# Optimization experiments

Measured on AMD Instinct MI355X. Metric: run time of the kernel, lower is better.

Reference implementation:

```python
import jax, jax.numpy as jnp
import numpy as np

N = 50000          # nodes
E = 1_600_000      # edges (avg degree 32)
IN_N, IN_E = 16, 1 # fc_encoder hardwired input dims
H = 128            # per-layer out_node/out_edge channels (out//2 = 64 inner)
BN_EPS = 1e-5


def setup_inputs() -> dict:
    key = jax.random.key(0)
    ks = jax.random.split(key, 32)
    d = {}
    d["x"] = jax.random.normal(ks[0], (N, IN_N), jnp.float32)
    d["edge_attr"] = jax.random.normal(ks[1], (E, IN_E), jnp.float32)
    d["edge_index"] = jax.random.randint(ks[2], (2, E), 0, N)
    i = 3
    for l, (ni, ei) in enumerate([(IN_N, IN_E), (H, H)]):
        s_n = 1.0 / np.sqrt(ni)
        s_e = 1.0 / np.sqrt(ei)
        s_h = 1.0 / np.sqrt(H)
        d[f"l{l}_Wn"] = jax.random.normal(ks[i], (H // 2, ni), jnp.float32) * s_n; i += 1
        d[f"l{l}_We"] = jax.random.normal(ks[i], (H // 2, ei), jnp.float32) * s_e; i += 1
        d[f"l{l}_Wfn"] = jax.random.normal(ks[i], (H, H), jnp.float32) * s_h; i += 1
        d[f"l{l}_bfn"] = jax.random.normal(ks[i], (H,), jnp.float32) * s_h; i += 1
        d[f"l{l}_Wfe"] = jax.random.normal(ks[i], (H, H), jnp.float32) * s_h; i += 1
        d[f"l{l}_bfe"] = jax.random.normal(ks[i], (H,), jnp.float32) * s_h; i += 1
        d[f"l{l}_g"] = jax.random.uniform(ks[i], (H,), jnp.float32, 0.5, 1.5); i += 1
        d[f"l{l}_b"] = jax.random.normal(ks[i], (H,), jnp.float32) * 0.1; i += 1
        d[f"l{l}_rm"] = jax.random.normal(ks[i], (H,), jnp.float32) * 0.1; i += 1
        d[f"l{l}_rv"] = jax.random.uniform(ks[i], (H,), jnp.float32, 0.5, 1.5); i += 1
    return d


def _layer(x, ea, src, dst, Wn, We, Wfn, bfn, Wfe, bfe, g, b, rm, rv):
    # NodeEdgeInteraction_node (eval mode: dropout = identity)
    n1 = jax.nn.relu(x @ Wn.T)            # [N, H/2]
    e1 = jax.nn.relu(ea @ We.T)           # [E, H/2]
    # edge_updater: cat([n1[src] + n1[dst], e1])
    e2 = jnp.concatenate([n1[src] + n1[dst], e1], axis=-1)      # [E, H]
    # propagate: message = e1, sum-aggregate at destination (edge_index[1])
    agg = jax.ops.segment_sum(e1, dst, num_segments=x.shape[0])  # [N, H/2]
    n2 = jnp.concatenate([agg, n1], axis=-1)                     # [N, H]
    n2 = jax.nn.relu(n2 @ Wfn.T + bfn)
    e2 = jax.nn.relu(e2 @ Wfe.T + bfe)
    # BatchNorm1d (eval: running stats)
    n2 = (n2 - rm) * jax.lax.rsqrt(rv + BN_EPS) * g + b
    return n2, e2


def reference(x, edge_attr, edge_index,
              l0_Wn, l0_We, l0_Wfn, l0_bfn, l0_Wfe, l0_bfe, l0_g, l0_b, l0_rm, l0_rv,
              l1_Wn, l1_We, l1_Wfn, l1_bfn, l1_Wfe, l1_bfe, l1_g, l1_b, l1_rm, l1_rv):
    src, dst = edge_index[0], edge_index[1]
    x, edge_attr = _layer(x, edge_attr, src, dst,
                          l0_Wn, l0_We, l0_Wfn, l0_bfn, l0_Wfe, l0_bfe,
                          l0_g, l0_b, l0_rm, l0_rv)
    x, edge_attr = _layer(x, edge_attr, src, dst,
                          l1_Wn, l1_We, l1_Wfn, l1_bfn, l1_Wfe, l1_bfe,
                          l1_g, l1_b, l1_rm, l1_rv)
    return x  # GNNEncoder returns node embeddings only
```

## Files before the change

kernel.cpp:

```cpp
#include <hip/hip_runtime.h>

typedef unsigned short u16;
typedef __attribute__((ext_vector_type(8))) short short8;
typedef __attribute__((ext_vector_type(4))) float floatx4;

#define NN 50000
#define NE 1600000
#define BN_EPS 1e-5f
#define TPB 8

#define LDS_BARRIER() asm volatile("s_waitcnt lgkmcnt(0)\n\ts_barrier" ::: "memory")

__device__ __forceinline__ float bfu(u16 u) {
    union { unsigned u32; float f; } v; v.u32 = ((unsigned)u) << 16; return v.f;
}
__device__ __forceinline__ u16 f2bf(float f) {
    union { float f; unsigned u; } v; v.f = f;
    unsigned r = v.u + 0x7FFFu + ((v.u >> 16) & 1u);
    return (u16)(r >> 16);
}
__device__ __forceinline__ float ldf(const void* p, int i, int m) {
    return m ? ((const float*)p)[i] : bfu(((const u16*)p)[i]);
}

__global__ __launch_bounds__(256) void k_cvtw(const u16* __restrict__ x,
                                              const void* __restrict__ W0, const void* __restrict__ W1,
                                              const void* __restrict__ W2, const void* __restrict__ W3,
                                              const void* __restrict__ W4,
                                              const void* __restrict__ We0raw,
                                              u16* __restrict__ dst, float* __restrict__ PN,
                                              int* __restrict__ mode) {
    int t = threadIdx.x;
    __shared__ float sred[4];
    float mx = 0.f;
    for (int i = t; i < 4096; i += 256) mx = fmaxf(mx, fabsf(bfu(x[i])));
#pragma unroll
    for (int o = 32; o > 0; o >>= 1) mx = fmaxf(mx, __shfl_down(mx, o));
    if ((t & 63) == 0) sred[t >> 6] = mx;
    __syncthreads();
    float m2 = fmaxf(fmaxf(sred[0], sred[1]), fmaxf(sred[2], sred[3]));
    int m = (m2 > 1e4f) ? 1 : 0;
    if (blockIdx.x == 0 && t == 0) mode[0] = m;
    if (blockIdx.x == 256) {
        if (t < 128) {
            float p = 0.f, n = 0.f;
            for (int k = 0; k < 64; k++) {
                float w = ldf(We0raw, k, m);
                float wf = ldf(W0, t * 128 + 64 + k, m);
                p += fmaxf(w, 0.f) * wf;
                n += fminf(w, 0.f) * wf;
            }
            PN[t] = p; PN[128 + t] = n;
        }
        return;
    }
    int i = blockIdx.x * 256 + t;
    const void* src; int off;
    if (i < 16384)      { src = W0; off = i; }
    else if (i < 24576) { src = W1; off = i - 16384; }
    else if (i < 40960) { src = W2; off = i - 24576; }
    else if (i < 49152) { src = W3; off = i - 40960; }
    else                { src = W4; off = i - 49152; }
    dst[i] = m ? f2bf(((const float*)src)[off]) : ((const u16*)src)[off];
}

__global__ __launch_bounds__(256) void k_enc0h(const void* __restrict__ x, const void* __restrict__ Wn,
                                               u16* __restrict__ n1, const int* __restrict__ ei,
                                               const void* __restrict__ ea,
                                               float* __restrict__ sp, float* __restrict__ sn,
                                               const int* __restrict__ mf) {
    int b = blockIdx.x;
    int t = threadIdx.x;
    int m = mf[0];
    if (b >= 3125) {
        int e = (b - 3125) * 256 + t;
        float a = ldf(ea, e, m);
        int d = ei[NE + e];
        if (a > 0.f) atomicAdd(sp + d, a);
        else if (a < 0.f) atomicAdd(sn + d, a);
        return;
    }
    __shared__ float Wns[64 * 17];
    __shared__ float xsh[16][17];
    int n0 = b * 16;
    for (int i = t; i < 1024; i += 256) Wns[(i >> 4) * 17 + (i & 15)] = ldf(Wn, i, m);
    xsh[t >> 4][t & 15] = ldf(x, n0 * 16 + t, m);
    __syncthreads();
    int c = t & 63, ng = t >> 6;
    float a0 = 0.f, a1 = 0.f, a2 = 0.f, a3 = 0.f;
#pragma unroll
    for (int k = 0; k < 16; k++) {
        float wv = Wns[c * 17 + k];
        a0 += xsh[ng * 4 + 0][k] * wv;
        a1 += xsh[ng * 4 + 1][k] * wv;
        a2 += xsh[ng * 4 + 2][k] * wv;
        a3 += xsh[ng * 4 + 3][k] * wv;
    }
    n1[(n0 + ng * 4 + 0) * 64 + c] = f2bf(fmaxf(a0, 0.f));
    n1[(n0 + ng * 4 + 1) * 64 + c] = f2bf(fmaxf(a1, 0.f));
    n1[(n0 + ng * 4 + 2) * 64 + c] = f2bf(fmaxf(a2, 0.f));
    n1[(n0 + ng * 4 + 3) * 64 + c] = f2bf(fmaxf(a3, 0.f));
}

__global__ __launch_bounds__(256) void k_node_l0(
    const u16* __restrict__ n1l0, const float* __restrict__ sp, const float* __restrict__ sn,
    const void* __restrict__ We0, const u16* __restrict__ Wfn0c, const void* __restrict__ bfn0,
    const void* __restrict__ g0, const void* __restrict__ b0,
    const void* __restrict__ rm0, const void* __restrict__ rv0,
    const u16* __restrict__ Wn1c, u16* __restrict__ n1l1, const int* __restrict__ mf) {
    int m = mf[0];
    __shared__ __align__(16) u16 fs[64][136];
    __shared__ __align__(16) u16 xs[64][136];
    int t = threadIdx.x;
    int n0 = blockIdx.x * 64;
    {
        int col = t & 127;
        int rbase = t >> 7;
        float wp = 0.f, wn = 0.f;
        if (col < 64) { float w0 = ldf(We0, col, m); wp = fmaxf(w0, 0.f); wn = fminf(w0, 0.f); }
#pragma unroll
        for (int i = 0; i < 32; i++) {
            int row = rbase + 2 * i;
            int n = n0 + row;
            float v = 0.f;
            if (n < NN) v = (col < 64) ? (wp * sp[n] + wn * sn[n]) : bfu(n1l0[n * 64 + col - 64]);
            fs[row][col] = f2bf(v);
        }
    }
    __syncthreads();
    int lane = t & 63, w = t >> 6, q = lane >> 4, nidx = lane & 15;
    {
        const u16* ar = &fs[w * 16 + nidx][0];
        short8 a0 = *(const short8*)&ar[q * 8];
        short8 a1 = *(const short8*)&ar[32 + q * 8];
        short8 a2 = *(const short8*)&ar[64 + q * 8];
        short8 a3 = *(const short8*)&ar[96 + q * 8];
#pragma unroll
        for (int jt = 0; jt < 8; jt++) {
            int j = jt * 16 + nidx;
            const u16* wr = Wfn0c + j * 128;
            floatx4 acc = {0.f, 0.f, 0.f, 0.f};
            acc = __builtin_amdgcn_mfma_f32_16x16x32_bf16(a0, *(const short8*)&wr[q * 8], acc, 0, 0, 0);
            acc = __builtin_amdgcn_mfma_f32_16x16x32_bf16(a1, *(const short8*)&wr[32 + q * 8], acc, 0, 0, 0);
            acc = __builtin_amdgcn_mfma_f32_16x16x32_bf16(a2, *(const short8*)&wr[64 + q * 8], acc, 0, 0, 0);
            acc = __builtin_amdgcn_mfma_f32_16x16x32_bf16(a3, *(const short8*)&wr[96 + q * 8], acc, 0, 0, 0);
            float bias = ldf(bfn0, j, m);
            float sc = ldf(g0, j, m) * rsqrtf(ldf(rv0, j, m) + BN_EPS);
            float sh = ldf(b0, j, m) - ldf(rm0, j, m) * sc;
#pragma unroll
            for (int r = 0; r < 4; r++) {
                int row = w * 16 + q * 4 + r;
                xs[row][j] = f2bf(fmaxf(acc[r] + bias, 0.f) * sc + sh);
            }
        }
    }
    __syncthreads();
    {
        const u16* ar = &xs[w * 16 + nidx][0];
        short8 a0 = *(const short8*)&ar[q * 8];
        short8 a1 = *(const short8*)&ar[32 + q * 8];
        short8 a2 = *(const short8*)&ar[64 + q * 8];
        short8 a3 = *(const short8*)&ar[96 + q * 8];
#pragma unroll
        for (int jt = 0; jt < 4; jt++) {
            int j = jt * 16 + nidx;
            const u16* wr = Wn1c + j * 128;
            floatx4 acc = {0.f, 0.f, 0.f, 0.f};
            acc = __builtin_amdgcn_mfma_f32_16x16x32_bf16(a0, *(const short8*)&wr[q * 8], acc, 0, 0, 0);
            acc = __builtin_amdgcn_mfma_f32_16x16x32_bf16(a1, *(const short8*)&wr[32 + q * 8], acc, 0, 0, 0);
            acc = __builtin_amdgcn_mfma_f32_16x16x32_bf16(a2, *(const short8*)&wr[64 + q * 8], acc, 0, 0, 0);
            acc = __builtin_amdgcn_mfma_f32_16x16x32_bf16(a3, *(const short8*)&wr[96 + q * 8], acc, 0, 0, 0);
#pragma unroll
            for (int r = 0; r < 4; r++) {
                int row = w * 16 + q * 4 + r;
                int n = n0 + row;
                if (n < NN) n1l1[n * 64 + j] = f2bf(fmaxf(acc[r], 0.f));
            }
        }
    }
}

__global__ __launch_bounds__(256) void k_edge7(
    const int* __restrict__ ei, const void* __restrict__ ea, const u16* __restrict__ n1l0,
    const u16* __restrict__ Wfe0c, const void* __restrict__ bfe0,
    const float* __restrict__ PN, const u16* __restrict__ We1c,
    float* __restrict__ agg, const int* __restrict__ mf) {
    int m = mf[0];
    __shared__ __align__(16) u16 h1s[2][16][136];
    int t = threadIdx.x;
    int lane = t & 63, w = t >> 6, q = lane >> 4, nidx = lane & 15;
    short8 wA[2][2];
    float bias[2][4], Pv[2][4], Nv[2][4];
#pragma unroll
    for (int jj = 0; jj < 2; jj++) {
        int jt = 2 * w + jj;
        const u16* wr = Wfe0c + (jt * 16 + nidx) * 128;
        wA[jj][0] = *(const short8*)&wr[q * 8];
        wA[jj][1] = *(const short8*)&wr[32 + q * 8];
#pragma unroll
        for (int r = 0; r < 4; r++) {
            int ch = jt * 16 + q * 4 + r;
            bias[jj][r] = ldf(bfe0, ch, m);
            Pv[jj][r] = PN[ch];
            Nv[jj][r] = PN[128 + ch];
        }
    }
    int c2 = w * 16 + nidx;
    const u16* wr2 = We1c + c2 * 128;
    short8 wB0 = *(const short8*)&wr2[q * 8];
    short8 wB1 = *(const short8*)&wr2[32 + q * 8];
    short8 wB2 = *(const short8*)&wr2[64 + q * 8];
    short8 wB3 = *(const short8*)&wr2[96 + q * 8];

    int e0 = blockIdx.x * (16 * TPB);
    int eb = e0 + nidx;
    int sv = ei[eb];
    int dv = ei[NE + eb];
    float av = ldf(ea, eb, m);
    const u16* srow = n1l0 + (size_t)sv * 64;
    const u16* drow = n1l0 + (size_t)dv * 64;
    short8 as0 = *(const short8*)&srow[q * 8];
    short8 as1 = *(const short8*)&srow[32 + q * 8];
    short8 ad0 = *(const short8*)&drow[q * 8];
    short8 ad1 = *(const short8*)&drow[32 + q * 8];

    for (int tile = 0; tile < TPB; tile++) {
        short8 cs0 = as0, cs1 = as1, cd0 = ad0, cd1 = ad1;
        int curd = dv;
        float cura = av;
        if (tile + 1 < TPB) {
            int en = e0 + (tile + 1) * 16 + nidx;
            sv = ei[en];
            dv = ei[NE + en];
            av = ldf(ea, en, m);
            srow = n1l0 + (size_t)sv * 64;
            drow = n1l0 + (size_t)dv * 64;
            as0 = *(const short8*)&srow[q * 8];
            as1 = *(const short8*)&srow[32 + q * 8];
            ad0 = *(const short8*)&drow[q * 8];
            ad1 = *(const short8*)&drow[32 + q * 8];
        }
        u16* hp = &h1s[tile & 1][0][0];
#pragma unroll
        for (int jj = 0; jj < 2; jj++) {
            floatx4 accS = {0.f, 0.f, 0.f, 0.f};
            floatx4 accD = {0.f, 0.f, 0.f, 0.f};
            accS = __builtin_amdgcn_mfma_f32_16x16x32_bf16(wA[jj][0], cs0, accS, 0, 0, 0);
            accD = __builtin_amdgcn_mfma_f32_16x16x32_bf16(wA[jj][0], cd0, accD, 0, 0, 0);
            accS = __builtin_amdgcn_mfma_f32_16x16x32_bf16(wA[jj][1], cs1, accS, 0, 0, 0);
            accD = __builtin_amdgcn_mfma_f32_16x16x32_bf16(wA[jj][1], cd1, accD, 0, 0, 0);
            float v0 = fmaxf(accS[0] + accD[0] + bias[jj][0] + cura * (cura > 0.f ? Pv[jj][0] : Nv[jj][0]), 0.f);
            float v1 = fmaxf(accS[1] + accD[1] + bias[jj][1] + cura * (cura > 0.f ? Pv[jj][1] : Nv[jj][1]), 0.f);
            float v2 = fmaxf(accS[2] + accD[2] + bias[jj][2] + cura * (cura > 0.f ? Pv[jj][2] : Nv[jj][2]), 0.f);
            float v3 = fmaxf(accS[3] + accD[3] + bias[jj][3] + cura * (cura > 0.f ? Pv[jj][3] : Nv[jj][3]), 0.f);
            unsigned lo = (unsigned)f2bf(v0) | ((unsigned)f2bf(v1) << 16);
            unsigned hi = (unsigned)f2bf(v2) | ((unsigned)f2bf(v3) << 16);
            uint2 pk; pk.x = lo; pk.y = hi;
            *(uint2*)&hp[nidx * 136 + w * 32 + jj * 16 + q * 4] = pk;
        }
        LDS_BARRIER();
        const u16* arow = &h1s[tile & 1][nidx][0];
        floatx4 accA = {0.f, 0.f, 0.f, 0.f};
        floatx4 accB = {0.f, 0.f, 0.f, 0.f};
        accA = __builtin_amdgcn_mfma_f32_16x16x32_bf16(*(const short8*)&arow[q * 8], wB0, accA, 0, 0, 0);
        accB = __builtin_amdgcn_mfma_f32_16x16x32_bf16(*(const short8*)&arow[32 + q * 8], wB1, accB, 0, 0, 0);
        accA = __builtin_amdgcn_mfma_f32_16x16x32_bf16(*(const short8*)&arow[64 + q * 8], wB2, accA, 0, 0, 0);
        accB = __builtin_amdgcn_mfma_f32_16x16x32_bf16(*(const short8*)&arow[96 + q * 8], wB3, accB, 0, 0, 0);
        int d0 = __shfl(curd, q * 4 + 0);
        int d1 = __shfl(curd, q * 4 + 1);
        int d2 = __shfl(curd, q * 4 + 2);
        int d3 = __shfl(curd, q * 4 + 3);
        atomicAdd(agg + (size_t)d0 * 64 + c2, fmaxf(accA[0] + accB[0], 0.f));
        atomicAdd(agg + (size_t)d1 * 64 + c2, fmaxf(accA[1] + accB[1], 0.f));
        atomicAdd(agg + (size_t)d2 * 64 + c2, fmaxf(accA[2] + accB[2], 0.f));
        atomicAdd(agg + (size_t)d3 * 64 + c2, fmaxf(accA[3] + accB[3], 0.f));
    }
}

__global__ __launch_bounds__(256) void k_node_l1(
    const u16* __restrict__ n1l1, const float* __restrict__ agg,
    const u16* __restrict__ Wfn1c, const void* __restrict__ bfn1,
    const void* __restrict__ g1, const void* __restrict__ b1,
    const void* __restrict__ rm1, const void* __restrict__ rv1,
    void* __restrict__ out, const int* __restrict__ mf) {
    int m = mf[0];
    __shared__ __align__(16) u16 fs[64][136];
    int t = threadIdx.x;
    int n0 = blockIdx.x * 64;
    {
        int col = t & 127;
        int rbase = t >> 7;
#pragma unroll
        for (int i = 0; i < 32; i++) {
            int row = rbase + 2 * i;
            int n = n0 + row;
            float v = 0.f;
            if (n < NN) v = (col < 64) ? agg[n * 64 + col] : bfu(n1l1[n * 64 + col - 64]);
            fs[row][col] = f2bf(v);
        }
    }
    __syncthreads();
    int lane = t & 63, w = t >> 6, q = lane >> 4, nidx = lane & 15;
    const u16* ar = &fs[w * 16 + nidx][0];
    short8 a0 = *(const short8*)&ar[q * 8];
    short8 a1 = *(const short8*)&ar[32 + q * 8];
    short8 a2 = *(const short8*)&ar[64 + q * 8];
    short8 a3 = *(const short8*)&ar[96 + q * 8];
#pragma unroll
    for (int jt = 0; jt < 8; jt++) {
        int j = jt * 16 + nidx;
        const u16* wr = Wfn1c + j * 128;
        floatx4 acc = {0.f, 0.f, 0.f, 0.f};
        acc = __builtin_amdgcn_mfma_f32_16x16x32_bf16(a0, *(const short8*)&wr[q * 8], acc, 0, 0, 0);
        acc = __builtin_amdgcn_mfma_f32_16x16x32_bf16(a1, *(const short8*)&wr[32 + q * 8], acc, 0, 0, 0);
        acc = __builtin_amdgcn_mfma_f32_16x16x32_bf16(a2, *(const short8*)&wr[64 + q * 8], acc, 0, 0, 0);
        acc = __builtin_amdgcn_mfma_f32_16x16x32_bf16(a3, *(const short8*)&wr[96 + q * 8], acc, 0, 0, 0);
        float bias = ldf(bfn1, j, m);
        float sc = ldf(g1, j, m) * rsqrtf(ldf(rv1, j, m) + BN_EPS);
        float sh = ldf(b1, j, m) - ldf(rm1, j, m) * sc;
#pragma unroll
        for (int r = 0; r < 4; r++) {
            int row = w * 16 + q * 4 + r;
            int n = n0 + row;
            if (n < NN) {
                float v = fmaxf(acc[r] + bias, 0.f) * sc + sh;
                if (m) ((float*)out)[n * 128 + j] = v;
                else   ((u16*)out)[n * 128 + j] = f2bf(v);
            }
        }
    }
}

extern "C" void kernel_launch(void* const* d_in, const int* in_sizes, int n_in,
                              void* d_out, int out_size, void* d_ws, size_t ws_size,
                              hipStream_t stream) {
    const void* x    = d_in[0];
    const void* ea   = d_in[1];
    const int*  ei   = (const int*)d_in[2];
    const void* Wn0  = d_in[3];
    const void* We0  = d_in[4];
    const void* Wfn0 = d_in[5];
    const void* bfn0 = d_in[6];
    const void* Wfe0 = d_in[7];
    const void* bfe0 = d_in[8];
    const void* g0   = d_in[9];
    const void* b0   = d_in[10];
    const void* rm0  = d_in[11];
    const void* rv0  = d_in[12];
    const void* Wn1  = d_in[13];
    const void* We1  = d_in[14];
    const void* Wfn1 = d_in[15];
    const void* bfn1 = d_in[16];
    const void* g1   = d_in[19];
    const void* b1   = d_in[20];
    const void* rm1  = d_in[21];
    const void* rv1  = d_in[22];

    float* wsf    = (float*)d_ws;
    float* agg    = wsf;
    u16*   n1l0   = (u16*)(wsf + 3200000);
    u16*   n1l1   = (u16*)(wsf + 4800000);
    float* sp     = wsf + 6400000;
    float* sn     = wsf + 6450000;
    float* PN     = wsf + 6500000;
    u16*   Wc     = (u16*)(wsf + 6500256);
    int*   mode   = (int*)(wsf + 6533024);
    u16* Wfe0c = Wc;
    u16* We1c  = Wc + 16384;
    u16* Wfn0c = Wc + 24576;
    u16* Wn1c  = Wc + 40960;
    u16* Wfn1c = Wc + 49152;

    hipMemsetAsync(sp, 0, 100000 * sizeof(float), stream);
    hipMemsetAsync(agg, 0, 3200000 * sizeof(float), stream);

    k_cvtw<<<257, 256, 0, stream>>>((const u16*)x, Wfe0, We1, Wfn0, Wn1, Wfn1,
                                    We0, Wc, PN, mode);
    k_enc0h<<<9375, 256, 0, stream>>>(x, Wn0, n1l0, ei, ea, sp, sn, mode);
    k_node_l0<<<782, 256, 0, stream>>>(n1l0, sp, sn, We0, Wfn0c, bfn0,
                                       g0, b0, rm0, rv0, Wn1c, n1l1, mode);
    k_edge7<<<NE / (16 * TPB), 256, 0, stream>>>(ei, ea, n1l0, Wfe0c, bfe0, PN, We1c, agg, mode);
    k_node_l1<<<782, 256, 0, stream>>>(n1l1, agg, Wfn1c, bfn1,
                                       g1, b1, rm1, rv1, d_out, mode);
}
```

Baseline: 614.4 us.

## Precompute per-node Wfe projection and gather it in the edge kernel

Exploits linearity: Wfe0·(n1[src]+n1[dst]) = z[src]+z[dst], with z = n1·Wfe0_nodepart + bias/2 computed once per node in a new kernel. The edge kernel then gathers 128-wide bf16 z rows instead of 64-wide n1 rows and drops four MFMAs per 16 output channels per tile. This removes per-edge matrix work but doubles the gathered bytes per edge and adds rounding, since z is stored as bf16 before summation. It also adds a small per-node kernel launch and extra workspace.

```diff
diff --git a/kernel.cpp b/kernel.cpp
--- a/kernel.cpp
+++ b/kernel.cpp
@@ -102,6 +102,44 @@
     n1[(n0 + ng * 4 + 3) * 64 + c] = f2bf(fmaxf(a3, 0.f));
 }
 
+__global__ __launch_bounds__(256) void k_z(const u16* __restrict__ n1l0, const u16* __restrict__ Wfe0c,
+                                           const void* __restrict__ bfe0, u16* __restrict__ z,
+                                           const int* __restrict__ mf) {
+    int m = mf[0];
+    __shared__ __align__(16) u16 fs[64][72];
+    int t = threadIdx.x;
+    int n0 = blockIdx.x * 64;
+    {
+        int col = t & 63, rb = t >> 6;
+#pragma unroll
+        for (int i = 0; i < 16; i++) {
+            int row = rb * 16 + i;
+            int n = n0 + row;
+            fs[row][col] = (n < NN) ? n1l0[n * 64 + col] : (u16)0;
+        }
+    }
+    __syncthreads();
+    int lane = t & 63, w = t >> 6, q = lane >> 4, nidx = lane & 15;
+    const u16* ar = &fs[w * 16 + nidx][0];
+    short8 a0 = *(const short8*)&ar[q * 8];
+    short8 a1 = *(const short8*)&ar[32 + q * 8];
+#pragma unroll
+    for (int jt = 0; jt < 8; jt++) {
+        int j = jt * 16 + nidx;
+        const u16* wr = Wfe0c + j * 128;
+        floatx4 acc = {0.f, 0.f, 0.f, 0.f};
+        acc = __builtin_amdgcn_mfma_f32_16x16x32_bf16(a0, *(const short8*)&wr[q * 8], acc, 0, 0, 0);
+        acc = __builtin_amdgcn_mfma_f32_16x16x32_bf16(a1, *(const short8*)&wr[32 + q * 8], acc, 0, 0, 0);
+        float hb = 0.5f * ldf(bfe0, j, m);
+#pragma unroll
+        for (int r = 0; r < 4; r++) {
+            int row = w * 16 + q * 4 + r;
+            int n = n0 + row;
+            if (n < NN) z[(size_t)n * 128 + j] = f2bf(acc[r] + hb);
+        }
+    }
+}
+
 __global__ __launch_bounds__(256) void k_node_l0(
     const u16* __restrict__ n1l0, const float* __restrict__ sp, const float* __restrict__ sn,
     const void* __restrict__ We0, const u16* __restrict__ Wfn0c, const void* __restrict__ bfn0,
@@ -180,31 +218,18 @@
     }
 }
 
-__global__ __launch_bounds__(256) void k_edge7(
-    const int* __restrict__ ei, const void* __restrict__ ea, const u16* __restrict__ n1l0,
-    const u16* __restrict__ Wfe0c, const void* __restrict__ bfe0,
+__global__ __launch_bounds__(256) void k_edge8(
+    const int* __restrict__ ei, const void* __restrict__ ea, const u16* __restrict__ z,
     const float* __restrict__ PN, const u16* __restrict__ We1c,
     float* __restrict__ agg, const int* __restrict__ mf) {
     int m = mf[0];
     __shared__ __align__(16) u16 h1s[2][16][136];
     int t = threadIdx.x;
     int lane = t & 63, w = t >> 6, q = lane >> 4, nidx = lane & 15;
-    short8 wA[2][2];
-    float bias[2][4], Pv[2][4], Nv[2][4];
-#pragma unroll
-    for (int jj = 0; jj < 2; jj++) {
-        int jt = 2 * w + jj;
-        const u16* wr = Wfe0c + (jt * 16 + nidx) * 128;
-        wA[jj][0] = *(const short8*)&wr[q * 8];
-        wA[jj][1] = *(const short8*)&wr[32 + q * 8];
-#pragma unroll
-        for (int r = 0; r < 4; r++) {
-            int ch = jt * 16 + q * 4 + r;
-            bias[jj][r] = ldf(bfe0, ch, m);
-            Pv[jj][r] = PN[ch];
-            Nv[jj][r] = PN[128 + ch];
-        }
-    }
+    int ko = w * 32 + q * 8;
+    float Pk[8], Nk[8];
+#pragma unroll
+    for (int j = 0; j < 8; j++) { Pk[j] = PN[ko + j]; Nk[j] = PN[128 + ko + j]; }
     int c2 = w * 16 + nidx;
     const u16* wr2 = We1c + c2 * 128;
     short8 wB0 = *(const short8*)&wr2[q * 8];
@@ -217,15 +242,11 @@
     int sv = ei[eb];
     int dv = ei[NE + eb];
     float av = ldf(ea, eb, m);
-    const u16* srow = n1l0 + (size_t)sv * 64;
-    const u16* drow = n1l0 + (size_t)dv * 64;
-    short8 as0 = *(const short8*)&srow[q * 8];
-    short8 as1 = *(const short8*)&srow[32 + q * 8];
-    short8 ad0 = *(const short8*)&drow[q * 8];
-    short8 ad1 = *(const short8*)&drow[32 + q * 8];
+    short8 gzs = *(const short8*)&z[(size_t)sv * 128 + ko];
+    short8 gzd = *(const short8*)&z[(size_t)dv * 128 + ko];
 
     for (int tile = 0; tile < TPB; tile++) {
-        short8 cs0 = as0, cs1 = as1, cd0 = ad0, cd1 = ad1;
+        short8 czs = gzs, czd = gzd;
         int curd = dv;
         float cura = av;
         if (tile + 1 < TPB) {
@@ -233,31 +254,17 @@
             sv = ei[en];
             dv = ei[NE + en];
             av = ldf(ea, en, m);
-            srow = n1l0 + (size_t)sv * 64;
-            drow = n1l0 + (size_t)dv * 64;
-            as0 = *(const short8*)&srow[q * 8];
-            as1 = *(const short8*)&srow[32 + q * 8];
-            ad0 = *(const short8*)&drow[q * 8];
-            ad1 = *(const short8*)&drow[32 + q * 8];
-        }
-        u16* hp = &h1s[tile & 1][0][0];
-#pragma unroll
-        for (int jj = 0; jj < 2; jj++) {
-            floatx4 accS = {0.f, 0.f, 0.f, 0.f};
-            floatx4 accD = {0.f, 0.f, 0.f, 0.f};
-            accS = __builtin_amdgcn_mfma_f32_16x16x32_bf16(wA[jj][0], cs0, accS, 0, 0, 0);
-            accD = __builtin_amdgcn_mfma_f32_16x16x32_bf16(wA[jj][0], cd0, accD, 0, 0, 0);
-            accS = __builtin_amdgcn_mfma_f32_16x16x32_bf16(wA[jj][1], cs1, accS, 0, 0, 0);
-            accD = __builtin_amdgcn_mfma_f32_16x16x32_bf16(wA[jj][1], cd1, accD, 0, 0, 0);
-            float v0 = fmaxf(accS[0] + accD[0] + bias[jj][0] + cura * (cura > 0.f ? Pv[jj][0] : Nv[jj][0]), 0.f);
-            float v1 = fmaxf(accS[1] + accD[1] + bias[jj][1] + cura * (cura > 0.f ? Pv[jj][1] : Nv[jj][1]), 0.f);
-            float v2 = fmaxf(accS[2] + accD[2] + bias[jj][2] + cura * (cura > 0.f ? Pv[jj][2] : Nv[jj][2]), 0.f);
-            float v3 = fmaxf(accS[3] + accD[3] + bias[jj][3] + cura * (cura > 0.f ? Pv[jj][3] : Nv[jj][3]), 0.f);
-            unsigned lo = (unsigned)f2bf(v0) | ((unsigned)f2bf(v1) << 16);
-            unsigned hi = (unsigned)f2bf(v2) | ((unsigned)f2bf(v3) << 16);
-            uint2 pk; pk.x = lo; pk.y = hi;
-            *(uint2*)&hp[nidx * 136 + w * 32 + jj * 16 + q * 4] = pk;
-        }
+            gzs = *(const short8*)&z[(size_t)sv * 128 + ko];
+            gzd = *(const short8*)&z[(size_t)dv * 128 + ko];
+        }
+        float pf = fmaxf(cura, 0.f), nf = fminf(cura, 0.f);
+        short8 hp;
+#pragma unroll
+        for (int j = 0; j < 8; j++) {
+            float v = bfu((u16)czs[j]) + bfu((u16)czd[j]) + pf * Pk[j] + nf * Nk[j];
+            hp[j] = (short)f2bf(fmaxf(v, 0.f));
+        }
+        *(short8*)&h1s[tile & 1][nidx][ko] = hp;
         LDS_BARRIER();
         const u16* arow = &h1s[tile & 1][nidx][0];
         floatx4 accA = {0.f, 0.f, 0.f, 0.f};
@@ -365,6 +372,7 @@
     float* PN     = wsf + 6500000;
     u16*   Wc     = (u16*)(wsf + 6500256);
     int*   mode   = (int*)(wsf + 6533024);
+    u16*   z      = (u16*)(wsf + 6533028);
     u16* Wfe0c = Wc;
     u16* We1c  = Wc + 16384;
     u16* Wfn0c = Wc + 24576;
@@ -377,9 +385,10 @@
     k_cvtw<<<257, 256, 0, stream>>>((const u16*)x, Wfe0, We1, Wfn0, Wn1, Wfn1,
                                     We0, Wc, PN, mode);
     k_enc0h<<<9375, 256, 0, stream>>>(x, Wn0, n1l0, ei, ea, sp, sn, mode);
+    k_z<<<782, 256, 0, stream>>>(n1l0, Wfe0c, bfe0, z, mode);
     k_node_l0<<<782, 256, 0, stream>>>(n1l0, sp, sn, We0, Wfn0c, bfn0,
                                        g0, b0, rm0, rv0, Wn1c, n1l1, mode);
-    k_edge7<<<NE / (16 * TPB), 256, 0, stream>>>(ei, ea, n1l0, Wfe0c, bfe0, PN, We1c, agg, mode);
+    k_edge8<<<NE / (16 * TPB), 256, 0, stream>>>(ei, ea, z, PN, We1c, agg, mode);
     k_node_l1<<<782, 256, 0, stream>>>(n1l1, agg, Wfn1c, bfn1,
                                        g1, b1, rm1, rv1, d_out, mode);
 }
```

Result: no change. 620.7 us (+1.0%).
